# Optimization experiments

Measured on AMD Instinct MI355X. Metric: run time of the kernel, lower is better.

## Reference

```python
import jax, jax.numpy as jnp
from jax import lax
import numpy as np

NUM_CLASSES = 80
STRIDES = (8, 16, 32)
CONF_THRE = 0.01
NMS_THRE = 0.65
TOPK = 500  # fixed pre-NMS candidate cap (jit-compatible stand-in for dynamic conf filter)


def setup_inputs() -> dict:
    key = jax.random.key(0)
    k8, k16, k32 = jax.random.split(key, 3)
    B, C = 8, 5 + NUM_CLASSES
    return {
        "out8": jax.random.normal(k8, (B, C, 160, 160), dtype=jnp.float32),
        "out16": jax.random.normal(k16, (B, C, 80, 80), dtype=jnp.float32),
        "out32": jax.random.normal(k32, (B, C, 40, 40), dtype=jnp.float32),
    }


def _decode_level(x, stride):
    # x: [B, C, H, W] -> decoded [B, H*W, C]
    B, C, H, W = x.shape
    x = x.reshape(B, C, H * W).transpose(0, 2, 1)  # [B, HW, C]
    yv, xv = jnp.meshgrid(jnp.arange(H), jnp.arange(W), indexing="ij")
    grid = jnp.stack([xv, yv], axis=-1).reshape(1, H * W, 2).astype(x.dtype)
    s = jnp.asarray(stride, x.dtype)
    xy = (x[..., 0:2] + grid) * s
    wh = jnp.exp(x[..., 2:4]) * s
    obj = jax.nn.sigmoid(x[..., 4:5])
    cls = jax.nn.sigmoid(x[..., 5:])
    return jnp.concatenate([xy, wh, obj, cls], axis=-1)


def _iou_one_vs_all(box, boxes):
    # box: [4] xyxy, boxes: [K,4] xyxy
    x1 = jnp.maximum(box[0], boxes[:, 0])
    y1 = jnp.maximum(box[1], boxes[:, 1])
    x2 = jnp.minimum(box[2], boxes[:, 2])
    y2 = jnp.minimum(box[3], boxes[:, 3])
    inter = jnp.maximum(x2 - x1, 0.0) * jnp.maximum(y2 - y1, 0.0)
    a1 = jnp.maximum(box[2] - box[0], 0.0) * jnp.maximum(box[3] - box[1], 0.0)
    a2 = jnp.maximum(boxes[:, 2] - boxes[:, 0], 0.0) * jnp.maximum(boxes[:, 3] - boxes[:, 1], 0.0)
    return inter / (a1 + a2 - inter + 1e-9)


def _nms_keep(boxes, valid, iou_thr):
    # boxes are pre-sorted by descending score; returns bool keep mask [K]
    K = boxes.shape[0]
    idx = jnp.arange(K)

    def body(i, state):
        keep, suppressed = state
        cur_ok = jnp.logical_not(suppressed[i])
        keep = keep.at[i].set(cur_ok)
        iou = _iou_one_vs_all(boxes[i], boxes)
        suppressed = suppressed | ((iou > iou_thr) & cur_ok & (idx > i))
        return keep, suppressed

    keep, _ = lax.fori_loop(0, K, body, (jnp.zeros(K, bool), jnp.logical_not(valid)))
    return keep


def _post_process_image(pred):
    # pred: [N, 5+num_classes] decoded, boxes already xyxy
    cls_scores = pred[:, 5:5 + NUM_CLASSES]
    class_conf = jnp.max(cls_scores, axis=1)
    class_pred = jnp.argmax(cls_scores, axis=1)
    obj = pred[:, 4]
    total = obj * class_conf  # NMS score, same as torchvision call
    masked = jnp.where(total >= CONF_THRE, total, -1.0)
    top_sc, top_i = lax.top_k(masked, TOPK)  # sorted descending
    boxes = pred[top_i, :4]
    obj_k = obj[top_i]
    cc_k = class_conf[top_i]
    lab_k = class_pred[top_i]
    valid = top_sc >= CONF_THRE
    # class-aware (batched) NMS via per-class coordinate offset, as torchvision does
    max_c = jnp.max(jnp.where(valid[:, None], boxes, 0.0)) + 1.0
    boxes_off = boxes + (lab_k.astype(boxes.dtype) * max_c)[:, None]
    keep = _nms_keep(boxes_off, valid, NMS_THRE)
    det = jnp.concatenate(
        [boxes, obj_k[:, None], cc_k[:, None], lab_k.astype(boxes.dtype)[:, None]], axis=1
    )  # [K, 7] = (x1,y1,x2,y2,obj,class_conf,class_id)
    return det * keep[:, None].astype(det.dtype)


def reference(out8, out16, out32):
    levels = [(out8, 8), (out16, 16), (out32, 32)]
    pred = jnp.concatenate([_decode_level(x, s) for x, s in levels], axis=1)  # [B, N, C]
    # cxcywh -> xyxy corners
    cx, cy, w, h = pred[..., 0], pred[..., 1], pred[..., 2], pred[..., 3]
    corners = jnp.stack([cx - w / 2, cy - h / 2, cx + w / 2, cy + h / 2], axis=-1)
    pred = jnp.concatenate([corners, pred[..., 4:]], axis=-1)
    return jax.vmap(_post_process_image)(pred)  # [B, TOPK, 7], zero-padded
```

## Files before the change

kernel.cpp:

```cpp
#include <hip/hip_runtime.h>

#define NPI    33600
#define KTOP   500
#define CAP    1024
#define KEY001 0xBC23D70Au
#define NGRP   1024
#define NIMG   8

__device__ __forceinline__ float sigmoidf_(float x) {
  return 1.0f / (1.0f + expf(-x));
}
__device__ __forceinline__ unsigned fkey(float f) {
  unsigned u = __float_as_uint(f);
  return (u & 0x80000000u) ? ~u : (u | 0x80000000u);
}

__global__ __launch_bounds__(256) void k_decode(
    const float* __restrict__ p8, const float* __restrict__ p16,
    const float* __restrict__ p32,
    unsigned* __restrict__ keys, float* __restrict__ dets,
    unsigned* __restrict__ hist2)
{
  const int b = blockIdx.y;
  const int t = blockIdx.x * 256 + threadIdx.x;
  const int a = t * 4;
  __shared__ unsigned lh[NGRP];
  for (int i = threadIdx.x; i < NGRP; i += 256) lh[i] = 0;
  __syncthreads();

  if (a < NPI) {
    const float* lvl; int j, W, HW, S;
    if (a < 25600)      { lvl = p8;  j = a;         W = 160; HW = 25600; S = 8;  }
    else if (a < 32000) { lvl = p16; j = a - 25600; W = 80;  HW = 6400;  S = 16; }
    else                { lvl = p32; j = a - 32000; W = 40;  HW = 1600;  S = 32; }
    const float* base = lvl + (size_t)b * 85 * HW + j;
    float4 t0 = *(const float4*)(base);
    float4 t1 = *(const float4*)(base + (size_t)1 * HW);
    float4 t2 = *(const float4*)(base + (size_t)2 * HW);
    float4 t3 = *(const float4*)(base + (size_t)3 * HW);
    float4 t4 = *(const float4*)(base + (size_t)4 * HW);
    float cc[4] = {-1.0f, -1.0f, -1.0f, -1.0f};
    int   lab[4] = {0, 0, 0, 0};
    #pragma unroll
    for (int c0 = 0; c0 < 80; c0 += 8) {
      float4 r[8];
      #pragma unroll
      for (int u = 0; u < 8; ++u)
        r[u] = *(const float4*)(base + (size_t)(5 + c0 + u) * HW);
      #pragma unroll
      for (int u = 0; u < 8; ++u) {
        float s;
        s = sigmoidf_(r[u].x); if (s > cc[0]) { cc[0] = s; lab[0] = c0 + u; }
        s = sigmoidf_(r[u].y); if (s > cc[1]) { cc[1] = s; lab[1] = c0 + u; }
        s = sigmoidf_(r[u].z); if (s > cc[2]) { cc[2] = s; lab[2] = c0 + u; }
        s = sigmoidf_(r[u].w); if (s > cc[3]) { cc[3] = s; lab[3] = c0 + u; }
      }
    }
    float e0[4] = {t0.x, t0.y, t0.z, t0.w};
    float e1[4] = {t1.x, t1.y, t1.z, t1.w};
    float e2[4] = {t2.x, t2.y, t2.z, t2.w};
    float e3[4] = {t3.x, t3.y, t3.z, t3.w};
    float e4[4] = {t4.x, t4.y, t4.z, t4.w};
    unsigned k4[4];
    float dv[7][4];
    #pragma unroll
    for (int e = 0; e < 4; ++e) {
      float obj = sigmoidf_(e4[e]);
      float tot = obj * cc[e];
      k4[e] = fkey(tot >= 0.01f ? tot : -1.0f);
      int jj = j + e;
      int gy = jj / W, gx = jj - gy * W;
      float fs = (float)S;
      float cx = (e0[e] + (float)gx) * fs;
      float cy = (e1[e] + (float)gy) * fs;
      float w  = expf(e2[e]) * fs;
      float h  = expf(e3[e]) * fs;
      dv[0][e] = cx - 0.5f * w; dv[1][e] = cy - 0.5f * h;
      dv[2][e] = cx + 0.5f * w; dv[3][e] = cy + 0.5f * h;
      dv[4][e] = obj; dv[5][e] = cc[e]; dv[6][e] = (float)lab[e];
    }
    *(uint4*)(keys + (size_t)b * NPI + a) = make_uint4(k4[0], k4[1], k4[2], k4[3]);
    const size_t P  = (size_t)NIMG * NPI;
    const size_t pa = (size_t)b * NPI + a;
    #pragma unroll
    for (int c = 0; c < 7; ++c)
      *(float4*)(dets + (size_t)c * P + pa) =
          make_float4(dv[c][0], dv[c][1], dv[c][2], dv[c][3]);
    #pragma unroll
    for (int e = 0; e < 4; ++e) atomicAdd(&lh[k4[e] >> 22], 1u);
  }
  __syncthreads();
  unsigned* gb = hist2 + (size_t)b * NGRP;
  for (int i = threadIdx.x; i < NGRP; i += 256) {
    unsigned v = lh[i];
    if (v) atomicAdd(&gb[i], v);
  }
}

__global__ __launch_bounds__(1024) void k_post(
    const unsigned* __restrict__ hist2, const unsigned* __restrict__ keys,
    const float* __restrict__ dets, float* __restrict__ out)
{
  const int b    = blockIdx.x;
  const int tid  = threadIdx.x;
  const int lane = tid & 63;
  const int wave = tid >> 6;

  __shared__ unsigned lh[NGRP];
  __shared__ unsigned sh_sub[4096];
  __shared__ unsigned sh_c64[64];
  __shared__ unsigned sh_G, sh_Chi10, sh_T, sh_Chi, sh_nA, sh_nB;
  __shared__ unsigned long long sh_cand[CAP];
  __shared__ float sh_det[KTOP][7];
  __shared__ float sh_box[KTOP][4];
  __shared__ unsigned sh_mask[KTOP * 16];
  __shared__ unsigned sh_inval[16];
  __shared__ unsigned sh_keep[16];
  __shared__ unsigned sh_wcA[16], sh_wcB[16];
  __shared__ float sh_red[16];
  __shared__ float sh_maxc;

  lh[tid] = hist2[(size_t)b * NGRP + tid];
  for (int i = tid; i < 4096; i += 1024) sh_sub[i] = 0;
  __syncthreads();
  if (tid < 64) {
    unsigned s = 0;
    #pragma unroll
    for (int k = 0; k < 16; ++k) s += lh[tid * 16 + k];
    sh_c64[tid] = s;
  }
  __syncthreads();
  if (tid == 0) {
    unsigned cum = 0; int C = 0;
    for (int g = 63; g >= 0; --g) {
      unsigned v = sh_c64[g];
      if (cum + v >= KTOP) { C = g; break; }
      cum += v;
    }
    int G = C * 16; unsigned chi = cum;
    for (int g = C * 16 + 15; g >= C * 16; --g) {
      unsigned v = lh[g];
      if (chi + v >= KTOP) { G = g; break; }
      chi += v;
    }
    sh_G = (unsigned)G; sh_Chi10 = chi;
    sh_nA = 0; sh_nB = 0;
  }
  __syncthreads();
  const unsigned G = sh_G;
  const unsigned* kb = keys + (size_t)b * NPI;

  for (int i = tid; i < NPI; i += 1024) {
    unsigned k = kb[i];
    if ((k >> 22) == G) atomicAdd(&sh_sub[(k >> 10) & 4095u], 1u);
  }
  __syncthreads();
  if (tid < 64) {
    unsigned s = 0;
    for (int k = 0; k < 64; ++k) s += sh_sub[tid * 64 + k];
    sh_c64[tid] = s;
  }
  __syncthreads();
  if (tid == 0) {
    unsigned c = sh_Chi10; int C2 = 0;
    for (int g = 63; g >= 0; --g) {
      unsigned v = sh_c64[g];
      if (c + v >= KTOP) { C2 = g; break; }
      c += v;
    }
    int T12 = C2 * 64;
    for (int t2 = C2 * 64 + 63; t2 >= C2 * 64; --t2) {
      unsigned v = sh_sub[t2];
      if (c + v >= KTOP) { T12 = t2; break; }
      c += v;
    }
    sh_T = (G << 12) | (unsigned)T12;
    sh_Chi = c;
  }
  __syncthreads();
  const unsigned T = sh_T, Chi = sh_Chi;
  const unsigned Bcap = CAP - Chi;

  for (int chunk = 0; chunk < 9; ++chunk) {
    int a0 = chunk * 4096 + tid * 4;
    unsigned kk[4]; bool iA[4], iB[4];
    bool act = (a0 < NPI);
    if (act) {
      uint4 kv = *(const uint4*)(kb + a0);
      kk[0] = kv.x; kk[1] = kv.y; kk[2] = kv.z; kk[3] = kv.w;
    } else { kk[0] = kk[1] = kk[2] = kk[3] = 0u; }
    #pragma unroll
    for (int e = 0; e < 4; ++e) {
      unsigned bin = kk[e] >> 10;
      iA[e] = act && (bin > T);
      iB[e] = act && (bin == T);
    }
    unsigned long long balA[4], balB[4];
    #pragma unroll
    for (int e = 0; e < 4; ++e) { balA[e] = __ballot(iA[e]); balB[e] = __ballot(iB[e]); }
    if (lane == 0) {
      unsigned sA = 0, sB = 0;
      #pragma unroll
      for (int e = 0; e < 4; ++e) { sA += (unsigned)__popcll(balA[e]); sB += (unsigned)__popcll(balB[e]); }
      sh_wcA[wave] = sA; sh_wcB[wave] = sB;
    }
    __syncthreads();
    unsigned pA = sh_nA, pB = sh_nB;
    for (int w2 = 0; w2 < wave; ++w2) { pA += sh_wcA[w2]; pB += sh_wcB[w2]; }
    unsigned long long lt = (1ULL << lane) - 1ULL;
    #pragma unroll
    for (int e = 0; e < 4; ++e) {
      pA += (unsigned)__popcll(balA[e] & lt);
      pB += (unsigned)__popcll(balB[e] & lt);
    }
    #pragma unroll
    for (int e = 0; e < 4; ++e) {
      unsigned long long packed =
          ((unsigned long long)kk[e] << 32) |
          (unsigned long long)(0xFFFFFFFFu - (unsigned)(a0 + e));
      if (iA[e]) { sh_cand[pA] = packed; ++pA; }
      if (iB[e]) { if (pB < Bcap) sh_cand[CAP - 1 - pB] = packed; ++pB; }
    }
    __syncthreads();
    if (tid == 0) {
      unsigned sA = 0, sB = 0;
      for (int w2 = 0; w2 < 16; ++w2) { sA += sh_wcA[w2]; sB += sh_wcB[w2]; }
      sh_nA += sA; sh_nB += sB;
    }
    __syncthreads();
  }
  {
    const unsigned nA  = sh_nA;
    const unsigned nBk = (sh_nB < Bcap) ? sh_nB : Bcap;
    for (int s = (int)nA + tid; s < (int)(CAP - nBk); s += 1024) sh_cand[s] = 0ULL;
  }
  __syncthreads();

  for (unsigned kk2 = 2; kk2 <= CAP; kk2 <<= 1) {
    for (unsigned jj = kk2 >> 1; jj > 0; jj >>= 1) {
      unsigned i = (unsigned)tid, p = i ^ jj;
      if (p > i) {
        unsigned long long x = sh_cand[i], y = sh_cand[p];
        bool desc = ((i & kk2) == 0);
        if ((x < y) == desc) { sh_cand[i] = y; sh_cand[p] = x; }
      }
      __syncthreads();
    }
  }

  bool validk = false;
  float contrib = -INFINITY;
  if (tid < KTOP) {
    unsigned long long v = sh_cand[tid];
    unsigned keyk = (unsigned)(v >> 32);
    int a = (int)(0xFFFFFFFFu - (unsigned)(v & 0xFFFFFFFFull));
    if (a < 0) a = 0;
    const size_t P  = (size_t)NIMG * NPI;
    const size_t pa = (size_t)b * NPI + (size_t)a;
    float det[7];
    #pragma unroll
    for (int c = 0; c < 7; ++c) det[c] = dets[(size_t)c * P + pa];
    #pragma unroll
    for (int c = 0; c < 7; ++c) sh_det[tid][c] = det[c];
    validk = (keyk >= KEY001);
    float m4 = fmaxf(fmaxf(det[0], det[1]), fmaxf(det[2], det[3]));
    contrib = validk ? m4 : 0.0f;
  }
  float r = contrib;
  #pragma unroll
  for (int off = 32; off > 0; off >>= 1) r = fmaxf(r, __shfl_xor(r, off));
  if (lane == 0) sh_red[wave] = r;
  unsigned long long bv = __ballot((tid < KTOP) && !validk);
  if (wave < 8 && lane == 0) {
    sh_inval[wave * 2]     = (unsigned)(bv & 0xFFFFFFFFull);
    sh_inval[wave * 2 + 1] = (unsigned)(bv >> 32);
  }
  __syncthreads();
  if (tid == 0) {
    float m = -INFINITY;
    for (int w2 = 0; w2 < 16; ++w2) m = fmaxf(m, sh_red[w2]);
    sh_maxc = m + 1.0f;
  }
  __syncthreads();
  const float maxc = sh_maxc;
  if (tid < KTOP) {
    float offb = sh_det[tid][6] * maxc;
    #pragma unroll
    for (int d = 0; d < 4; ++d) sh_box[tid][d] = sh_det[tid][d] + offb;
  }
  __syncthreads();

  for (int task = tid; task < KTOP * 16; task += 1024) {
    int i = task % KTOP;
    int w = task / KTOP;
    int jbase = w * 32;
    unsigned bits = 0u;
    if (jbase + 31 > i) {
      float ix1 = sh_box[i][0], iy1 = sh_box[i][1], ix2 = sh_box[i][2], iy2 = sh_box[i][3];
      float a1 = fmaxf(ix2 - ix1, 0.0f) * fmaxf(iy2 - iy1, 0.0f);
      #pragma unroll 4
      for (int jj = 0; jj < 32; ++jj) {
        int j = jbase + jj;
        if (j < KTOP && j > i) {
          float jx1 = sh_box[j][0], jy1 = sh_box[j][1];
          float jx2 = sh_box[j][2], jy2 = sh_box[j][3];
          float iw = fminf(ix2, jx2) - fmaxf(ix1, jx1);
          float ih = fminf(iy2, jy2) - fmaxf(iy1, jy1);
          float inter = fmaxf(iw, 0.0f) * fmaxf(ih, 0.0f);
          float a2 = fmaxf(jx2 - jx1, 0.0f) * fmaxf(jy2 - jy1, 0.0f);
          if (inter > 0.65f * (a1 + a2 - inter + 1e-9f)) bits |= (1u << jj);
        }
      }
    }
    sh_mask[i * 16 + w] = bits;
  }
  __syncthreads();

  if (tid < 64) {
    unsigned sup   = (lane < 16) ? sh_inval[lane] : 0u;
    unsigned keepw = 0u;
    unsigned cur = (unsigned)__builtin_amdgcn_readlane((int)sup, 0);
    unsigned mA = (lane < 16) ? sh_mask[0 * 16 + lane] : 0u;
    unsigned mB = (lane < 16) ? sh_mask[1 * 16 + lane] : 0u;
    for (int i = 0; i < KTOP; i += 2) {
      bool ok = ((cur >> (i & 31)) & 1u) == 0u;
      if (ok) {
        sup |= mA;
        if (lane == (i >> 5)) keepw |= (1u << (i & 31));
      }
      cur = (unsigned)__builtin_amdgcn_readlane((int)sup, (i + 1) >> 5);
      mA = (lane < 16 && (i + 2) < KTOP) ? sh_mask[(i + 2) * 16 + lane] : 0u;
      bool ok2 = ((cur >> ((i + 1) & 31)) & 1u) == 0u;
      if (ok2) {
        sup |= mB;
        if (lane == ((i + 1) >> 5)) keepw |= (1u << ((i + 1) & 31));
      }
      cur = (unsigned)__builtin_amdgcn_readlane((int)sup, (i + 2) >> 5);
      mB = (lane < 16 && (i + 3) < KTOP) ? sh_mask[(i + 3) * 16 + lane] : 0u;
    }
    if (lane < 16) sh_keep[lane] = keepw;
  }
  __syncthreads();

  for (int x = tid; x < KTOP * 7; x += 1024) {
    int k = x / 7, c = x - k * 7;
    float keepf = ((sh_keep[k >> 5] >> (k & 31)) & 1u) ? 1.0f : 0.0f;
    out[(size_t)b * (KTOP * 7) + x] = sh_det[k][c] * keepf;
  }
}

extern "C" void kernel_launch(void* const* d_in, const int* in_sizes, int n_in,
                              void* d_out, int out_size, void* d_ws, size_t ws_size,
                              hipStream_t stream) {
  const float* p8  = (const float*)d_in[0];
  const float* p16 = (const float*)d_in[1];
  const float* p32 = (const float*)d_in[2];
  float* out = (float*)d_out;
  unsigned* hist2 = (unsigned*)d_ws;
  unsigned* keys  = hist2 + (size_t)NIMG * NGRP;
  float*    dets  = (float*)(keys + (size_t)NIMG * NPI);

  hipMemsetAsync(hist2, 0, (size_t)NIMG * NGRP * 4, stream);
  k_decode<<<dim3(33, NIMG), 256, 0, stream>>>(p8, p16, p32, keys, dets, hist2);
  k_post<<<dim3(NIMG), 1024, 0, stream>>>(hist2, keys, dets, out);
}
```

Before: 250.0 us.

## Halve decode work per thread and restructure top-K selection and IoU mask build

The decode kernel now handles two anchors per thread with float2 loads across twice as many blocks, aiming for more parallelism and latency hiding. In the post kernel, candidate compaction uses per-wave contiguous ranges with a count pass, removing the per-chunk block barriers. The bitonic sort is replaced by a rank-by-counting sort using readlane broadcasts. The IoU mask build moves to SoA shared arrays with precomputed areas and broadcasts column boxes via readlane. Together these cut barrier-heavy steps in a single-block-per-image kernel, at the cost of extra global key reads and an O(n^2) rank computation.

Measured after the change: 254.1 us. About the same (+1.6%).

```diff
diff --git a/kernel.cpp b/kernel.cpp
--- a/kernel.cpp
+++ b/kernel.cpp
@@ -6,6 +6,7 @@
 #define KEY001 0xBC23D70Au
 #define NGRP   1024
 #define NIMG   8
+#define GPW    525
 
 __device__ __forceinline__ float sigmoidf_(float x) {
   return 1.0f / (1.0f + expf(-x));
@@ -13,6 +14,14 @@
 __device__ __forceinline__ unsigned fkey(float f) {
   unsigned u = __float_as_uint(f);
   return (u & 0x80000000u) ? ~u : (u | 0x80000000u);
+}
+__device__ __forceinline__ unsigned long long rdlane64(unsigned long long v, int l) {
+  unsigned lo = (unsigned)__builtin_amdgcn_readlane((int)(unsigned)(v & 0xFFFFFFFFull), l);
+  unsigned hi = (unsigned)__builtin_amdgcn_readlane((int)(unsigned)(v >> 32), l);
+  return ((unsigned long long)hi << 32) | lo;
+}
+__device__ __forceinline__ float rdlanef(float v, int l) {
+  return __uint_as_float((unsigned)__builtin_amdgcn_readlane((int)__float_as_uint(v), l));
 }
 
 __global__ __launch_bounds__(256) void k_decode(
@@ -23,7 +32,7 @@
 {
   const int b = blockIdx.y;
   const int t = blockIdx.x * 256 + threadIdx.x;
-  const int a = t * 4;
+  const int a = t * 2;
   __shared__ unsigned lh[NGRP];
   for (int i = threadIdx.x; i < NGRP; i += 256) lh[i] = 0;
   __syncthreads();
@@ -34,40 +43,37 @@
     else if (a < 32000) { lvl = p16; j = a - 25600; W = 80;  HW = 6400;  S = 16; }
     else                { lvl = p32; j = a - 32000; W = 40;  HW = 1600;  S = 32; }
     const float* base = lvl + (size_t)b * 85 * HW + j;
-    float4 t0 = *(const float4*)(base);
-    float4 t1 = *(const float4*)(base + (size_t)1 * HW);
-    float4 t2 = *(const float4*)(base + (size_t)2 * HW);
-    float4 t3 = *(const float4*)(base + (size_t)3 * HW);
-    float4 t4 = *(const float4*)(base + (size_t)4 * HW);
-    float cc[4] = {-1.0f, -1.0f, -1.0f, -1.0f};
-    int   lab[4] = {0, 0, 0, 0};
-    #pragma unroll
+    float2 t0 = *(const float2*)(base);
+    float2 t1 = *(const float2*)(base + (size_t)1 * HW);
+    float2 t2 = *(const float2*)(base + (size_t)2 * HW);
+    float2 t3 = *(const float2*)(base + (size_t)3 * HW);
+    float2 t4 = *(const float2*)(base + (size_t)4 * HW);
+    float cc[2] = {-1.0f, -1.0f};
+    int   lab[2] = {0, 0};
     for (int c0 = 0; c0 < 80; c0 += 8) {
-      float4 r[8];
+      float2 r[8];
       #pragma unroll
       for (int u = 0; u < 8; ++u)
-        r[u] = *(const float4*)(base + (size_t)(5 + c0 + u) * HW);
+        r[u] = *(const float2*)(base + (size_t)(5 + c0 + u) * HW);
       #pragma unroll
       for (int u = 0; u < 8; ++u) {
         float s;
         s = sigmoidf_(r[u].x); if (s > cc[0]) { cc[0] = s; lab[0] = c0 + u; }
         s = sigmoidf_(r[u].y); if (s > cc[1]) { cc[1] = s; lab[1] = c0 + u; }
-        s = sigmoidf_(r[u].z); if (s > cc[2]) { cc[2] = s; lab[2] = c0 + u; }
-        s = sigmoidf_(r[u].w); if (s > cc[3]) { cc[3] = s; lab[3] = c0 + u; }
       }
     }
-    float e0[4] = {t0.x, t0.y, t0.z, t0.w};
-    float e1[4] = {t1.x, t1.y, t1.z, t1.w};
-    float e2[4] = {t2.x, t2.y, t2.z, t2.w};
-    float e3[4] = {t3.x, t3.y, t3.z, t3.w};
-    float e4[4] = {t4.x, t4.y, t4.z, t4.w};
-    unsigned k4[4];
-    float dv[7][4];
-    #pragma unroll
-    for (int e = 0; e < 4; ++e) {
+    float e0[2] = {t0.x, t0.y};
+    float e1[2] = {t1.x, t1.y};
+    float e2[2] = {t2.x, t2.y};
+    float e3[2] = {t3.x, t3.y};
+    float e4[2] = {t4.x, t4.y};
+    unsigned k2[2];
+    float dv[7][2];
+    #pragma unroll
+    for (int e = 0; e < 2; ++e) {
       float obj = sigmoidf_(e4[e]);
       float tot = obj * cc[e];
-      k4[e] = fkey(tot >= 0.01f ? tot : -1.0f);
+      k2[e] = fkey(tot >= 0.01f ? tot : -1.0f);
       int jj = j + e;
       int gy = jj / W, gx = jj - gy * W;
       float fs = (float)S;
@@ -79,15 +85,14 @@
       dv[2][e] = cx + 0.5f * w; dv[3][e] = cy + 0.5f * h;
       dv[4][e] = obj; dv[5][e] = cc[e]; dv[6][e] = (float)lab[e];
     }
-    *(uint4*)(keys + (size_t)b * NPI + a) = make_uint4(k4[0], k4[1], k4[2], k4[3]);
+    *(uint2*)(keys + (size_t)b * NPI + a) = make_uint2(k2[0], k2[1]);
     const size_t P  = (size_t)NIMG * NPI;
     const size_t pa = (size_t)b * NPI + a;
     #pragma unroll
     for (int c = 0; c < 7; ++c)
-      *(float4*)(dets + (size_t)c * P + pa) =
-          make_float4(dv[c][0], dv[c][1], dv[c][2], dv[c][3]);
-    #pragma unroll
-    for (int e = 0; e < 4; ++e) atomicAdd(&lh[k4[e] >> 22], 1u);
+      *(float2*)(dets + (size_t)c * P + pa) = make_float2(dv[c][0], dv[c][1]);
+    atomicAdd(&lh[k2[0] >> 22], 1u);
+    atomicAdd(&lh[k2[1] >> 22], 1u);
   }
   __syncthreads();
   unsigned* gb = hist2 + (size_t)b * NGRP;
@@ -109,10 +114,11 @@
   __shared__ unsigned lh[NGRP];
   __shared__ unsigned sh_sub[4096];
   __shared__ unsigned sh_c64[64];
-  __shared__ unsigned sh_G, sh_Chi10, sh_T, sh_Chi, sh_nA, sh_nB;
-  __shared__ unsigned long long sh_cand[CAP];
+  __shared__ unsigned sh_G, sh_T;
+  __shared__ __align__(16) unsigned long long sh_cand[CAP];
+  __shared__ unsigned long long sh_sorted[KTOP];
   __shared__ float sh_det[KTOP][7];
-  __shared__ float sh_box[KTOP][4];
+  __shared__ float sbx1[512], sby1[512], sbx2[512], sby2[512], sar[512];
   __shared__ unsigned sh_mask[KTOP * 16];
   __shared__ unsigned sh_inval[16];
   __shared__ unsigned sh_keep[16];
@@ -143,17 +149,22 @@
       if (chi + v >= KTOP) { G = g; break; }
       chi += v;
     }
-    sh_G = (unsigned)G; sh_Chi10 = chi;
-    sh_nA = 0; sh_nB = 0;
+    sh_G = (unsigned)G;
+    sh_c64[0] = chi;
   }
   __syncthreads();
   const unsigned G = sh_G;
   const unsigned* kb = keys + (size_t)b * NPI;
 
-  for (int i = tid; i < NPI; i += 1024) {
-    unsigned k = kb[i];
-    if ((k >> 22) == G) atomicAdd(&sh_sub[(k >> 10) & 4095u], 1u);
-  }
+  for (int g = tid; g < NPI / 4; g += 1024) {
+    uint4 kv = ((const uint4*)kb)[g];
+    unsigned kk[4] = {kv.x, kv.y, kv.z, kv.w};
+    #pragma unroll
+    for (int e = 0; e < 4; ++e)
+      if ((kk[e] >> 22) == G) atomicAdd(&sh_sub[(kk[e] >> 10) & 4095u], 1u);
+  }
+  __syncthreads();
+  unsigned chi10 = sh_c64[0];
   __syncthreads();
   if (tid < 64) {
     unsigned s = 0;
@@ -162,7 +173,7 @@
   }
   __syncthreads();
   if (tid == 0) {
-    unsigned c = sh_Chi10; int C2 = 0;
+    unsigned c = chi10; int C2 = 0;
     for (int g = 63; g >= 0; --g) {
       unsigned v = sh_c64[g];
       if (c + v >= KTOP) { C2 = g; break; }
@@ -175,89 +186,102 @@
       c += v;
     }
     sh_T = (G << 12) | (unsigned)T12;
-    sh_Chi = c;
-  }
-  __syncthreads();
-  const unsigned T = sh_T, Chi = sh_Chi;
-  const unsigned Bcap = CAP - Chi;
-
-  for (int chunk = 0; chunk < 9; ++chunk) {
-    int a0 = chunk * 4096 + tid * 4;
-    unsigned kk[4]; bool iA[4], iB[4];
-    bool act = (a0 < NPI);
-    if (act) {
-      uint4 kv = *(const uint4*)(kb + a0);
-      kk[0] = kv.x; kk[1] = kv.y; kk[2] = kv.z; kk[3] = kv.w;
-    } else { kk[0] = kk[1] = kk[2] = kk[3] = 0u; }
+  }
+  __syncthreads();
+  const unsigned T = sh_T;
+
+  unsigned runA = 0, runB = 0;
+  for (int it = 0; it < 9; ++it) {
+    int gl = it * 64 + lane;
+    bool act = (gl < GPW);
+    int g = wave * GPW + gl;
+    uint4 kv = act ? ((const uint4*)kb)[g] : make_uint4(0, 0, 0, 0);
+    unsigned kk[4] = {kv.x, kv.y, kv.z, kv.w};
+    #pragma unroll
+    for (int e = 0; e < 4; ++e) {
+      unsigned bin = kk[e] >> 10;
+      runA += (unsigned)__popcll(__ballot(act && (bin > T)));
+      runB += (unsigned)__popcll(__ballot(act && (bin == T)));
+    }
+  }
+  if (lane == 0) { sh_wcA[wave] = runA; sh_wcB[wave] = runB; }
+  __syncthreads();
+  unsigned pA = 0, pB = 0, nA = 0, nBtot = 0;
+  #pragma unroll
+  for (int w2 = 0; w2 < 16; ++w2) {
+    unsigned va = sh_wcA[w2], vb = sh_wcB[w2];
+    if (w2 < wave) { pA += va; pB += vb; }
+    nA += va; nBtot += vb;
+  }
+  const unsigned Bcap = CAP - nA;
+  const unsigned nBk  = (nBtot < Bcap) ? nBtot : Bcap;
+  const int nTot = (int)(nA + nBk);
+
+  for (int it = 0; it < 9; ++it) {
+    int gl = it * 64 + lane;
+    bool act = (gl < GPW);
+    int g = wave * GPW + gl;
+    uint4 kv = act ? ((const uint4*)kb)[g] : make_uint4(0, 0, 0, 0);
+    unsigned kk[4] = {kv.x, kv.y, kv.z, kv.w};
+    bool iA[4], iB[4];
+    unsigned long long balA[4], balB[4];
     #pragma unroll
     for (int e = 0; e < 4; ++e) {
       unsigned bin = kk[e] >> 10;
       iA[e] = act && (bin > T);
       iB[e] = act && (bin == T);
-    }
-    unsigned long long balA[4], balB[4];
-    #pragma unroll
-    for (int e = 0; e < 4; ++e) { balA[e] = __ballot(iA[e]); balB[e] = __ballot(iB[e]); }
-    if (lane == 0) {
-      unsigned sA = 0, sB = 0;
-      #pragma unroll
-      for (int e = 0; e < 4; ++e) { sA += (unsigned)__popcll(balA[e]); sB += (unsigned)__popcll(balB[e]); }
-      sh_wcA[wave] = sA; sh_wcB[wave] = sB;
-    }
-    __syncthreads();
-    unsigned pA = sh_nA, pB = sh_nB;
-    for (int w2 = 0; w2 < wave; ++w2) { pA += sh_wcA[w2]; pB += sh_wcB[w2]; }
+      balA[e] = __ballot(iA[e]);
+      balB[e] = __ballot(iB[e]);
+    }
     unsigned long long lt = (1ULL << lane) - 1ULL;
+    unsigned pAl = pA, pBl = pB;
     #pragma unroll
     for (int e = 0; e < 4; ++e) {
-      pA += (unsigned)__popcll(balA[e] & lt);
-      pB += (unsigned)__popcll(balB[e] & lt);
+      pAl += (unsigned)__popcll(balA[e] & lt);
+      pBl += (unsigned)__popcll(balB[e] & lt);
     }
     #pragma unroll
     for (int e = 0; e < 4; ++e) {
+      int a0 = g * 4 + e;
       unsigned long long packed =
           ((unsigned long long)kk[e] << 32) |
-          (unsigned long long)(0xFFFFFFFFu - (unsigned)(a0 + e));
-      if (iA[e]) { sh_cand[pA] = packed; ++pA; }
-      if (iB[e]) { if (pB < Bcap) sh_cand[CAP - 1 - pB] = packed; ++pB; }
-    }
-    __syncthreads();
-    if (tid == 0) {
-      unsigned sA = 0, sB = 0;
-      for (int w2 = 0; w2 < 16; ++w2) { sA += sh_wcA[w2]; sB += sh_wcB[w2]; }
-      sh_nA += sA; sh_nB += sB;
-    }
-    __syncthreads();
-  }
+          (unsigned long long)(0xFFFFFFFFu - (unsigned)a0);
+      if (iA[e]) { sh_cand[pAl] = packed; ++pAl; }
+      if (iB[e]) { if (pBl < Bcap) sh_cand[nA + pBl] = packed; ++pBl; }
+      pA += (unsigned)__popcll(balA[e]);
+      pB += (unsigned)__popcll(balB[e]);
+    }
+  }
+  __syncthreads();
+
   {
-    const unsigned nA  = sh_nA;
-    const unsigned nBk = (sh_nB < Bcap) ? sh_nB : Bcap;
-    for (int s = (int)nA + tid; s < (int)(CAP - nBk); s += 1024) sh_cand[s] = 0ULL;
-  }
-  __syncthreads();
-
-  for (unsigned kk2 = 2; kk2 <= CAP; kk2 <<= 1) {
-    for (unsigned jj = kk2 >> 1; jj > 0; jj >>= 1) {
-      unsigned i = (unsigned)tid, p = i ^ jj;
-      if (p > i) {
-        unsigned long long x = sh_cand[i], y = sh_cand[p];
-        bool desc = ((i & kk2) == 0);
-        if ((x < y) == desc) { sh_cand[i] = y; sh_cand[p] = x; }
+    unsigned long long cnd[16];
+    #pragma unroll
+    for (int k = 0; k < 16; ++k) cnd[k] = sh_cand[64 * k + lane];
+    unsigned long long mine = sh_cand[tid];
+    int rank = 0;
+    #pragma unroll
+    for (int k = 0; k < 16; ++k) {
+      int base0 = 64 * k;
+      if (base0 < nTot) {
+        int lim = nTot - base0; if (lim > 64) lim = 64;
+        for (int l = 0; l < lim; ++l)
+          rank += (rdlane64(cnd[k], l) > mine) ? 1 : 0;
       }
-      __syncthreads();
-    }
-  }
+    }
+    if (tid < nTot && rank < KTOP) sh_sorted[rank] = mine;
+  }
+  __syncthreads();
 
   bool validk = false;
   float contrib = -INFINITY;
+  float det[7];
   if (tid < KTOP) {
-    unsigned long long v = sh_cand[tid];
+    unsigned long long v = sh_sorted[tid];
     unsigned keyk = (unsigned)(v >> 32);
     int a = (int)(0xFFFFFFFFu - (unsigned)(v & 0xFFFFFFFFull));
-    if (a < 0) a = 0;
     const size_t P  = (size_t)NIMG * NPI;
     const size_t pa = (size_t)b * NPI + (size_t)a;
-    float det[7];
     #pragma unroll
     for (int c = 0; c < 7; ++c) det[c] = dets[(size_t)c * P + pa];
     #pragma unroll
@@ -283,36 +307,57 @@
   }
   __syncthreads();
   const float maxc = sh_maxc;
-  if (tid < KTOP) {
-    float offb = sh_det[tid][6] * maxc;
-    #pragma unroll
-    for (int d = 0; d < 4; ++d) sh_box[tid][d] = sh_det[tid][d] + offb;
-  }
-  __syncthreads();
-
-  for (int task = tid; task < KTOP * 16; task += 1024) {
-    int i = task % KTOP;
-    int w = task / KTOP;
-    int jbase = w * 32;
-    unsigned bits = 0u;
-    if (jbase + 31 > i) {
-      float ix1 = sh_box[i][0], iy1 = sh_box[i][1], ix2 = sh_box[i][2], iy2 = sh_box[i][3];
-      float a1 = fmaxf(ix2 - ix1, 0.0f) * fmaxf(iy2 - iy1, 0.0f);
-      #pragma unroll 4
-      for (int jj = 0; jj < 32; ++jj) {
-        int j = jbase + jj;
-        if (j < KTOP && j > i) {
-          float jx1 = sh_box[j][0], jy1 = sh_box[j][1];
-          float jx2 = sh_box[j][2], jy2 = sh_box[j][3];
-          float iw = fminf(ix2, jx2) - fmaxf(ix1, jx1);
-          float ih = fminf(iy2, jy2) - fmaxf(iy1, jy1);
-          float inter = fmaxf(iw, 0.0f) * fmaxf(ih, 0.0f);
-          float a2 = fmaxf(jx2 - jx1, 0.0f) * fmaxf(jy2 - jy1, 0.0f);
-          if (inter > 0.65f * (a1 + a2 - inter + 1e-9f)) bits |= (1u << jj);
+  if (tid < 512) {
+    if (tid < KTOP) {
+      float offb = det[6] * maxc;
+      float x1 = det[0] + offb, y1 = det[1] + offb;
+      float x2 = det[2] + offb, y2 = det[3] + offb;
+      sbx1[tid] = x1; sby1[tid] = y1; sbx2[tid] = x2; sby2[tid] = y2;
+      sar[tid] = fmaxf(x2 - x1, 0.0f) * fmaxf(y2 - y1, 0.0f);
+    } else {
+      sbx1[tid] = 0.0f; sby1[tid] = 0.0f; sbx2[tid] = 0.0f; sby2[tid] = 0.0f;
+      sar[tid] = 0.0f;
+    }
+  }
+  __syncthreads();
+
+  {
+    float cb1[8], cb2[8], cb3[8], cb4[8], car[8];
+    #pragma unroll
+    for (int k = 0; k < 8; ++k) {
+      int j = 64 * k + lane;
+      cb1[k] = sbx1[j]; cb2[k] = sby1[j]; cb3[k] = sbx2[j]; cb4[k] = sby2[j];
+      car[k] = sar[j];
+    }
+    const int w = wave, jbase = w * 32, q = w >> 1, l0 = (w & 1) * 32;
+    float jb1 = cb1[0], jb2 = cb2[0], jb3 = cb3[0], jb4 = cb4[0], jb5 = car[0];
+    #pragma unroll
+    for (int k = 1; k < 8; ++k)
+      if (q == k) { jb1 = cb1[k]; jb2 = cb2[k]; jb3 = cb3[k]; jb4 = cb4[k]; jb5 = car[k]; }
+    for (int it = 0; it < 8; ++it) {
+      int i = it * 64 + lane;
+      unsigned bits = 0u;
+      if (jbase + 31 > it * 64) {
+        float ix1 = sbx1[i], iy1 = sby1[i], ix2 = sbx2[i], iy2 = sby2[i];
+        float a1 = sar[i];
+        #pragma unroll
+        for (int jj = 0; jj < 32; ++jj) {
+          int j = jbase + jj;
+          float jx1 = rdlanef(jb1, l0 + jj);
+          float jy1 = rdlanef(jb2, l0 + jj);
+          float jx2 = rdlanef(jb3, l0 + jj);
+          float jy2 = rdlanef(jb4, l0 + jj);
+          float a2  = rdlanef(jb5, l0 + jj);
+          if (j < KTOP && j > i) {
+            float iw = fminf(ix2, jx2) - fmaxf(ix1, jx1);
+            float ih = fminf(iy2, jy2) - fmaxf(iy1, jy1);
+            float inter = fmaxf(iw, 0.0f) * fmaxf(ih, 0.0f);
+            if (inter > 0.65f * (a1 + a2 - inter + 1e-9f)) bits |= (1u << jj);
+          }
         }
       }
-    }
-    sh_mask[i * 16 + w] = bits;
+      if (i < KTOP) sh_mask[i * 16 + w] = bits;
+    }
   }
   __syncthreads();
 
@@ -361,6 +406,6 @@
   float*    dets  = (float*)(keys + (size_t)NIMG * NPI);
 
   hipMemsetAsync(hist2, 0, (size_t)NIMG * NGRP * 4, stream);
-  k_decode<<<dim3(33, NIMG), 256, 0, stream>>>(p8, p16, p32, keys, dets, hist2);
+  k_decode<<<dim3(66, NIMG), 256, 0, stream>>>(p8, p16, p32, keys, dets, hist2);
   k_post<<<dim3(NIMG), 1024, 0, stream>>>(hist2, keys, dets, out);
 }
```
